# Performance work log

Hardware: AMD Instinct MI355X
Metric: run time of the kernel (lower is better)

Reference implementation:

```python
import jax, jax.numpy as jnp
import numpy as np

N, F, C, H, E, G, L = 50000, 128, 64, 4, 500000, 32, 4
EPS = 1e-5
NEG_SLOPE = 0.2


def setup_inputs() -> dict:
    key = jax.random.key(0)
    ks = jax.random.split(key, 16)
    x = jax.random.normal(ks[0], (N, F), dtype=jnp.float32)
    edge_index = jax.random.randint(ks[1], (2, E), 0, N, dtype=jnp.int64)
    batch = jnp.sort(jax.random.randint(ks[2], (N,), 0, G, dtype=jnp.int64))
    s = 0.05
    params = {
        'Wp': jax.random.normal(ks[3], (F, C), jnp.float32) * s,          # initial_proj (no bias)
        'Wl': jax.random.normal(ks[4], (L, C, H * C), jnp.float32) * s,   # GATv2 lin_l per layer
        'bl': jax.random.normal(ks[5], (L, H * C), jnp.float32) * s,
        'Wr': jax.random.normal(ks[6], (L, C, H * C), jnp.float32) * s,   # GATv2 lin_r per layer
        'br': jax.random.normal(ks[7], (L, H * C), jnp.float32) * s,
        'att': jax.random.normal(ks[8], (L, H, C), jnp.float32) * s,      # attention vector per head
        'cb': jax.random.normal(ks[9], (L, C), jnp.float32) * s,          # conv output bias (concat=False)
        'ln_w': jnp.ones((L, C), jnp.float32),                            # pyg LayerNorm affine
        'ln_b': jnp.zeros((L, C), jnp.float32),
        'Wh': jax.random.normal(ks[10], (C, 1), jnp.float32) * s,         # head
        'bh': jnp.zeros((1,), jnp.float32),
    }
    return {'x': x, 'edge_index': edge_index, 'batch': batch, **params}


def _gatv2(x, src, dst, Wl, bl, Wr, br, att, cb):
    # x: [N, C] -> per-head projections [N, H, C]
    xl = (x @ Wl + bl).reshape(N, H, C)
    xr = (x @ Wr + br).reshape(N, H, C)
    # edge-wise GATv2 scores: leaky_relu(x_i + x_j) . att   -> [E, H]
    e = jax.nn.leaky_relu(xl[src] + xr[dst], NEG_SLOPE)
    score = jnp.einsum('ehc,hc->eh', e, att)
    # segment softmax over incoming edges of each destination node
    m = jax.ops.segment_max(score, dst, num_segments=N)[dst]
    p = jnp.exp(score - m)
    denom = jax.ops.segment_sum(p, dst, num_segments=N)[dst]
    alpha = p / denom                                     # [E, H]
    msg = xl[src] * alpha[..., None]                      # [E, H, C]
    out = jax.ops.segment_sum(msg, dst, num_segments=N)   # [N, H, C]
    return out.mean(axis=1) + cb                          # concat=False: head mean + bias


def _graph_norm(x, w, b):
    # pyg.nn.LayerNorm mode='graph' with batch=None: normalize over ALL elements
    xc = x - x.mean()
    std = jnp.sqrt(xc.var())
    return (xc / (std + EPS)) * w + b


def reference(x, edge_index, batch, Wp, Wl, bl, Wr, br, att, cb, ln_w, ln_b, Wh, bh):
    src, dst = edge_index[0], edge_index[1]
    h = x @ Wp
    for l in range(L):
        h = _gatv2(h, src, dst, Wl[l], bl[l], Wr[l], br[l], att[l], cb[l])
        h = jax.nn.selu(_graph_norm(h, ln_w[l], ln_b[l]))
    # global mean pool over graphs
    counts = jax.ops.segment_sum(jnp.ones((N,), h.dtype), batch, num_segments=G)
    pooled = jax.ops.segment_sum(h, batch, num_segments=G) / jnp.maximum(counts, 1.0)[:, None]
    return (pooled @ Wh + bh).squeeze(-1)  # [G]
```

## Files before the change

### kernel.cpp

```cpp
#include <hip/hip_runtime.h>
#include <hip/hip_bf16.h>
#include <hip/hip_fp8.h>
#include <math.h>

#define NN 50000
#define FIN 128
#define CC 64
#define HH 4
#define HC 256
#define EE 500000
#define GG 32
#define LL 4

typedef __hip_bfloat16 bf16;
typedef __attribute__((ext_vector_type(2))) float f2;
typedef __attribute__((ext_vector_type(8))) short s8v;
typedef __attribute__((ext_vector_type(4))) float f4v;

__device__ __forceinline__ float b2f(bf16 v){ return __bfloat162float(v); }
__device__ __forceinline__ bf16 f2b(float v){ return __float2bfloat16(v); }
__device__ __forceinline__ void unpack2(unsigned u, float& a, float& b){
  union { unsigned q; float f; } x, y;
  x.q = u << 16; y.q = u & 0xffff0000u; a = x.f; b = y.f;
}
__device__ __forceinline__ f2 unpackf2(unsigned u){
  union { unsigned q; float f; } x, y;
  x.q = u << 16; y.q = u & 0xffff0000u;
  f2 r; r.x = x.f; r.y = y.f; return r;
}
__device__ __forceinline__ f2 maxf2(f2 a, f2 b){
#if __has_builtin(__builtin_elementwise_max)
  return __builtin_elementwise_max(a, b);
#else
  f2 r; r.x = fmaxf(a.x, b.x); r.y = fmaxf(a.y, b.y); return r;
#endif
}
__device__ __forceinline__ float clamp4(float v){ return fminf(fmaxf(v, -1e4f), 1e4f); }
__device__ __forceinline__ unsigned pack2bf(float a, float b){
  bf16 x = f2b(clamp4(a)), y = f2b(clamp4(b));
  unsigned short ux = *(unsigned short*)&x, uy = *(unsigned short*)&y;
  return (unsigned)ux | ((unsigned)uy << 16);
}
__device__ __forceinline__ unsigned f4_to_fp8x4(float a, float b, float c, float d){
  a = fminf(fmaxf(a, -240.f), 240.f);
  b = fminf(fmaxf(b, -240.f), 240.f);
  c = fminf(fmaxf(c, -240.f), 240.f);
  d = fminf(fmaxf(d, -240.f), 240.f);
#if __has_builtin(__builtin_amdgcn_cvt_pk_fp8_f32)
  int p = 0;
  p = __builtin_amdgcn_cvt_pk_fp8_f32(a, b, p, false);
  p = __builtin_amdgcn_cvt_pk_fp8_f32(c, d, p, true);
  return (unsigned)p;
#else
  __hip_fp8_e4m3 qa(a), qb(b), qc(c), qd(d);
  return (unsigned)qa.__x | ((unsigned)qb.__x << 8) | ((unsigned)qc.__x << 16) | ((unsigned)qd.__x << 24);
#endif
}
__device__ __forceinline__ void fp8x4_to_f2(unsigned u, f2& lo, f2& hi){
#if __has_builtin(__builtin_amdgcn_cvt_pk_f32_fp8)
  lo = __builtin_amdgcn_cvt_pk_f32_fp8((int)u, false);
  hi = __builtin_amdgcn_cvt_pk_f32_fp8((int)u, true);
#else
  __hip_fp8_e4m3 q0, q1, q2, q3;
  q0.__x = u & 0xff; q1.__x = (u >> 8) & 0xff; q2.__x = (u >> 16) & 0xff; q3.__x = (u >> 24) & 0xff;
  lo.x = (float)q0; lo.y = (float)q1; hi.x = (float)q2; hi.y = (float)q3;
#endif
}
__device__ __forceinline__ float selu_f(float y){
  const float SS = 1.0507009873554805f, SA = 1.6732632423543772f;
  return y > 0.f ? SS*y : SS*SA*(__expf(y) - 1.f);
}
__device__ __forceinline__ int ld_i(const void* p, int i, int w8){
  if (w8) return (int)((const long long*)p)[i];
  return ((const int*)p)[i];
}
__device__ __forceinline__ void stats_inline(const float* __restrict__ partials, float& mu, float& inv){
  float s1 = 0.f, s2 = 0.f;
  #pragma unroll 8
  for (int i = 0; i < 64; ++i){ s1 += partials[i]; s2 += partials[64 + i]; }
  float cnt = (float)NN * 64.f;
  mu = s1 / cnt;
  float var = s2 / cnt - mu*mu;
  if (!(var > 0.f)) var = 0.f;
  inv = 1.0f / (sqrtf(var) + 1e-5f);
}

__global__ __launch_bounds__(256) void k_setup(
    const void* ei, const void* batch,
    const void* Wp, const void* Wl, const void* bl, const void* Wr, const void* br,
    const void* att, const void* cb, const void* lnw, const void* lnb,
    const void* Wh, const void* bh,
    float* dst, int* deg, float* pooled, int* flags, short* apack){
  int b = blockIdx.x;
  int t = threadIdx.x;
  const unsigned short* lw = (const unsigned short*)lnw;
  int f32 = (lw[0] == 0x0000 && lw[1] == 0x3F80) ? 1 : 0;
  if (b < 560){
    int i = b*256 + t;
    if (i < 143169){
      const void* src; int idx;
      if      (i < 8192)   { src = Wp;  idx = i; }
      else if (i < 73728)  { src = Wl;  idx = i - 8192; }
      else if (i < 74752)  { src = bl;  idx = i - 73728; }
      else if (i < 140288) { src = Wr;  idx = i - 74752; }
      else if (i < 141312) { src = br;  idx = i - 140288; }
      else if (i < 142336) { src = att; idx = i - 141312; }
      else if (i < 142592) { src = cb;  idx = i - 142336; }
      else if (i < 142848) { src = lnw; idx = i - 142592; }
      else if (i < 143104) { src = lnb; idx = i - 142848; }
      else if (i < 143168) { src = Wh;  idx = i - 143104; }
      else                 { src = bh;  idx = 0; }
      dst[i] = f32 ? ((const float*)src)[idx] : b2f(((const bf16*)src)[idx]);
    }
  } else if (b < 756){
    int i = (b - 560)*256 + t;
    if (i < NN) deg[i] = 0;
  } else if (b == 756){
    for (int i = t; i < GG*64; i += 256) pooled[i] = 0.f;
    if (t < 64){
      int lane = t;
      const int* w  = (const int*)ei;
      const int* wb = (const int*)batch;
      int bad_e = (lane < 32) ? (w[2*(lane*15625) + 1] != 0) : 0;
      int bad_b = (lane < 32) ? (wb[25001 + 2*lane] != 0) : 0;
      unsigned long long me = __ballot(bad_e);
      unsigned long long mb = __ballot(bad_b);
      if (lane == 0){
        flags[0] = (me == 0ULL) ? 1 : 0;
        flags[1] = (mb == 0ULL) ? 1 : 0;
        flags[2] = f32;
      }
    }
  } else {
    int i2 = (b - 757)*256 + t;
    int l   = i2 >> 15;
    int rem = i2 & 32767;
    int ct  = rem >> 10;
    int rem2 = rem & 1023;
    int kh  = rem2 >> 9;
    int li  = (rem2 >> 3) & 63;
    int j   = rem2 & 7;
    int k   = kh*32 + ((li >> 4) << 3) + j;
    int c   = (ct << 4) + (li & 15);
    const void* Wsrc = (c < 256) ? Wl : Wr;
    int cc = c & 255;
    size_t idx = ((size_t)l*64 + k)*256 + cc;
    float v = f32 ? ((const float*)Wsrc)[idx] : b2f(((const bf16*)Wsrc)[idx]);
    bf16 bv = f2b(v);
    apack[i2] = *(short*)&bv;
  }
}

__global__ __launch_bounds__(256) void k_hist(const void* __restrict__ ei, int* __restrict__ deg,
                                              const int* __restrict__ flags){
  int e = blockIdx.x*256 + threadIdx.x;
  if (e < EE){
    int d = ld_i(ei, EE + e, flags[0]);
    if ((unsigned)d < NN) atomicAdd(&deg[d], 1);
  }
}

__global__ __launch_bounds__(256) void k_scan1(const int* __restrict__ deg, int* __restrict__ off,
                                               int* __restrict__ btot){
  int t = threadIdx.x;
  int i = blockIdx.x*256 + t;
  int v = (i < NN) ? deg[i] : 0;
  int incl = v;
  #pragma unroll
  for (int dl = 1; dl < 64; dl <<= 1){
    int u = __shfl_up(incl, dl, 64);
    if ((t & 63) >= dl) incl += u;
  }
  __shared__ int wt[4];
  if ((t & 63) == 63) wt[t >> 6] = incl;
  __syncthreads();
  int base = 0;
  for (int ww = 0; ww < (t >> 6); ++ww) base += wt[ww];
  incl += base;
  if (i < NN) off[i + 1] = incl;
  if (t == 255) btot[blockIdx.x] = incl;
}

__global__ __launch_bounds__(256) void k_scan2(const int* __restrict__ btot, int* __restrict__ boff, int nb){
  int t = threadIdx.x;
  int v = (t < nb) ? btot[t] : 0;
  int incl = v;
  #pragma unroll
  for (int dl = 1; dl < 64; dl <<= 1){
    int u = __shfl_up(incl, dl, 64);
    if ((t & 63) >= dl) incl += u;
  }
  __shared__ int wt[4];
  if ((t & 63) == 63) wt[t >> 6] = incl;
  __syncthreads();
  int base = 0;
  for (int ww = 0; ww < (t >> 6); ++ww) base += wt[ww];
  incl += base;
  if (t < 256) boff[t] = incl - v;
}

__global__ __launch_bounds__(256) void k_scan3(int* __restrict__ off, int* __restrict__ cursor,
                                               const int* __restrict__ deg, const int* __restrict__ boff){
  int i = blockIdx.x*256 + threadIdx.x;
  if (i >= NN) return;
  int v = off[i + 1] + boff[i >> 8];
  off[i + 1] = v;
  cursor[i] = v - deg[i];
  if (i == 0) off[0] = 0;
}

__global__ __launch_bounds__(256) void k_scatter_gb(const void* __restrict__ ei, int* __restrict__ cursor,
                                                    int* __restrict__ ssrc, const void* __restrict__ batch,
                                                    int* __restrict__ gstart, const int* __restrict__ flags){
  int b = blockIdx.x;
  if (b < 1954){
    int e = b*256 + threadIdx.x;
    if (e < EE){
      int f = flags[0];
      int s = ld_i(ei, e, f);
      int d = ld_i(ei, EE + e, f);
      if ((unsigned)d < NN && (unsigned)s < NN){
        int p = atomicAdd(&cursor[d], 1);
        ssrc[p] = s << 8;
      }
    }
  } else {
    int i = (b - 1954)*256 + threadIdx.x;
    if (i >= NN) return;
    int f = flags[1];
    int bb = ld_i(batch, i, f);
    bb = min(max(bb, 0), GG - 1);
    if (i == 0){ for (int q = 0; q <= bb; ++q) gstart[q] = 0; }
    else {
      int pb = ld_i(batch, i - 1, f);
      pb = min(max(pb, 0), GG - 1);
      for (int q = pb + 1; q <= bb; ++q) gstart[q] = i;
    }
    if (i == NN - 1){ for (int q = bb + 1; q <= GG; ++q) gstart[q] = NN; }
  }
}

__global__ __launch_bounds__(256) void k_proj(const void* __restrict__ xraw, const float* __restrict__ Wp32,
                                              float* __restrict__ h, const int* __restrict__ flags){
  __shared__ float xs[64*128];
  __shared__ float wsm[128*64];
  int t = threadIdx.x;
  int r0 = blockIdx.x * 64;
  int rows = NN - r0; if (rows > 64) rows = 64;
  const float4* gw = (const float4*)Wp32;
  #pragma unroll
  for (int i = 0; i < 8; ++i) ((float4*)wsm)[i*256 + t] = gw[i*256 + t];
  int f32 = flags[2];
  #pragma unroll
  for (int i = 0; i < 8; ++i){
    int p = i*256 + t;
    int r = p >> 5, kq = p & 31;
    float4 v = make_float4(0.f,0.f,0.f,0.f);
    if (r < rows){
      if (f32) v = ((const float4*)xraw)[(size_t)(r0 + r)*32 + kq];
      else {
        uint2 u = ((const uint2*)xraw)[(size_t)(r0 + r)*32 + kq];
        unpack2(u.x, v.x, v.y); unpack2(u.y, v.z, v.w);
      }
    }
    *(float4*)&xs[r*128 + kq*4] = v;
  }
  __syncthreads();
  int tx = t & 15, ty = t >> 4;
  int c0 = tx*4, rr0 = ty*4;
  float acc[4][4] = {{0.f}};
  for (int k = 0; k < 128; k += 4){
    float4 xv[4];
    #pragma unroll
    for (int i = 0; i < 4; ++i) xv[i] = *(const float4*)&xs[(rr0 + i)*128 + k];
    const float* xf = (const float*)xv;
    #pragma unroll
    for (int m = 0; m < 4; ++m){
      float4 wv = *(const float4*)&wsm[(k + m)*64 + c0];
      #pragma unroll
      for (int i = 0; i < 4; ++i){
        float xm = xf[i*4 + m];
        acc[i][0] = fmaf(xm, wv.x, acc[i][0]);
        acc[i][1] = fmaf(xm, wv.y, acc[i][1]);
        acc[i][2] = fmaf(xm, wv.z, acc[i][2]);
        acc[i][3] = fmaf(xm, wv.w, acc[i][3]);
      }
    }
  }
  #pragma unroll
  for (int i = 0; i < 4; ++i){
    int r = rr0 + i;
    if (r < rows){
      float4 o;
      o.x = clamp4(acc[i][0]); o.y = clamp4(acc[i][1]);
      o.z = clamp4(acc[i][2]); o.w = clamp4(acc[i][3]);
      *(float4*)&h[(size_t)(r0 + r)*64 + c0] = o;
    }
  }
}

__global__ __launch_bounds__(256) void k_gemm2m(const float* __restrict__ h,
    const s8v* __restrict__ apack,
    const float* __restrict__ bl, const float* __restrict__ br,
    unsigned char* __restrict__ xl8, bf16* __restrict__ xr,
    const float* __restrict__ partials, const float* __restrict__ lnw, const float* __restrict__ lnb,
    int apply){
  __shared__ short buf[64*264];
  int t = threadIdx.x;
  int r0 = blockIdx.x * 64;
  int rows = NN - r0; if (rows > 64) rows = 64;
  float mu = 0.f, inv = 0.f;
  if (apply) stats_inline(partials, mu, inv);
  #pragma unroll
  for (int i = 0; i < 4; ++i){
    int p = i*256 + t;
    int r = p >> 4, kq = p & 15;
    uint2 pk; pk.x = 0u; pk.y = 0u;
    if (r < rows){
      float4 v = ((const float4*)h)[(size_t)(r0 + r)*16 + kq];
      if (apply){
        float4 w4 = *(const float4*)(lnw + kq*4);
        float4 b4 = *(const float4*)(lnb + kq*4);
        v.x = selu_f((v.x - mu)*inv*w4.x + b4.x);
        v.y = selu_f((v.y - mu)*inv*w4.y + b4.y);
        v.z = selu_f((v.z - mu)*inv*w4.z + b4.z);
        v.w = selu_f((v.w - mu)*inv*w4.w + b4.w);
      }
      pk.x = pack2bf(v.x, v.y);
      pk.y = pack2bf(v.z, v.w);
    }
    *(uint2*)&buf[r*264 + kq*4] = pk;
  }
  __syncthreads();
  int wave = t >> 6, lane = t & 63;
  int n = lane & 15, q = lane >> 4;
  int rowb = wave * 16;
  s8v bf0 = *(const s8v*)&buf[(rowb + n)*264 + q*8];
  s8v bf1 = *(const s8v*)&buf[(rowb + n)*264 + 32 + q*8];
  __syncthreads();
  {
    unsigned* ubuf = (unsigned*)buf;
    #pragma unroll 4
    for (int cc = 0; cc < 16; ++cc){
      s8v a0 = apack[cc*128 + lane];
      s8v a1 = apack[cc*128 + 64 + lane];
      f4v acc = {0.f, 0.f, 0.f, 0.f};
      acc = __builtin_amdgcn_mfma_f32_16x16x32_bf16(a0, bf0, acc, 0, 0, 0);
      acc = __builtin_amdgcn_mfma_f32_16x16x32_bf16(a1, bf1, acc, 0, 0, 0);
      int colh = (cc << 4) + (q << 2);
      float4 bb = *(const float4*)&bl[colh];
      ubuf[(rowb + n)*132 + (colh >> 2)] =
          f4_to_fp8x4(acc[0] + bb.x, acc[1] + bb.y, acc[2] + bb.z, acc[3] + bb.w);
    }
    __syncthreads();
    #pragma unroll
    for (int i = 0; i < 16; ++i){
      int idx = i*256 + t;
      int row = idx >> 6, colu = idx & 63;
      if (row < rows){
        unsigned v = ubuf[row*132 + colu];
        ((unsigned*)xl8)[((size_t)(r0 + row))*64 + colu] = v;
      }
    }
    __syncthreads();
  }
  {
    #pragma unroll 4
    for (int cc = 0; cc < 16; ++cc){
      int ct = 16 + cc;
      s8v a0 = apack[ct*128 + lane];
      s8v a1 = apack[ct*128 + 64 + lane];
      f4v acc = {0.f, 0.f, 0.f, 0.f};
      acc = __builtin_amdgcn_mfma_f32_16x16x32_bf16(a0, bf0, acc, 0, 0, 0);
      acc = __builtin_amdgcn_mfma_f32_16x16x32_bf16(a1, bf1, acc, 0, 0, 0);
      int colh = (cc << 4) + (q << 2);
      float4 bb = *(const float4*)&br[colh];
      uint2 pk;
      pk.x = pack2bf(acc[0] + bb.x, acc[1] + bb.y);
      pk.y = pack2bf(acc[2] + bb.z, acc[3] + bb.w);
      *(uint2*)&buf[(rowb + n)*264 + colh] = pk;
    }
    __syncthreads();
    #pragma unroll
    for (int i = 0; i < 16; ++i){
      int idx = i*256 + t;
      int row = idx >> 6, col = idx & 63;
      if (row < rows){
        uint2 v = *(const uint2*)&buf[row*264 + col*4];
        *(uint2*)&xr[((size_t)(r0 + row))*256 + col*4] = v;
      }
    }
  }
}

__global__ __launch_bounds__(256) void k_gat(const unsigned char* __restrict__ xl8, const bf16* __restrict__ xr,
    const int* __restrict__ off, const int* __restrict__ ssrc,
    const float* __restrict__ att, const float* __restrict__ cbp,
    float* __restrict__ out, float2* __restrict__ nstat){
  int t = threadIdx.x;
  int wave = t >> 6, lane = t & 63;
  int d = blockIdx.x*4 + wave;
  if (d >= NN) return;
  int s0 = off[d], s1 = off[d + 1];
  int head = lane >> 4;
  int c4 = (lane & 15) * 4;

  float4 av4 = *(const float4*)(att + head*64 + c4);
  f2 av01; av01.x = av4.x; av01.y = av4.y;
  f2 av23; av23.x = av4.z; av23.y = av4.w;
  uint2 ur = *(const uint2*)(xr + (size_t)d * 256 + lane*4);
  f2 r01 = unpackf2(ur.x), r23 = unpackf2(ur.y);
  const float NS = 0.2f;

  float denom = 0.f;
  f2 m01; m01.x = 0.f; m01.y = 0.f;
  f2 m23; m23.x = 0.f; m23.y = 0.f;
  int e = s0;
  for (; e + 1 < s1; e += 2){
    int ofa = ssrc[e];
    int ofb = ssrc[e + 1];
    unsigned ua = *(const unsigned*)(xl8 + (size_t)(unsigned)ofa + lane*4);
    unsigned ub = *(const unsigned*)(xl8 + (size_t)(unsigned)ofb + lane*4);
    f2 xa01, xa23, xb01, xb23;
    fp8x4_to_f2(ua, xa01, xa23);
    fp8x4_to_f2(ub, xb01, xb23);
    f2 ta01 = xa01 + r01, ta23 = xa23 + r23;
    f2 tb01 = xb01 + r01, tb23 = xb23 + r23;
    ta01 = maxf2(ta01, ta01*NS); ta23 = maxf2(ta23, ta23*NS);
    tb01 = maxf2(tb01, tb01*NS); tb23 = maxf2(tb23, tb23*NS);
    f2 sa2 = av01*ta01 + av23*ta23;
    f2 sb2 = av01*tb01 + av23*tb23;
    float sa = sa2.x + sa2.y;
    float sb = sb2.x + sb2.y;
    sa += __shfl_xor(sa, 1, 64); sb += __shfl_xor(sb, 1, 64);
    sa += __shfl_xor(sa, 2, 64); sb += __shfl_xor(sb, 2, 64);
    sa += __shfl_xor(sa, 4, 64); sb += __shfl_xor(sb, 4, 64);
    sa += __shfl_xor(sa, 8, 64); sb += __shfl_xor(sb, 8, 64);
    float pa = __expf(fminf(sa, 30.f));
    float pb = __expf(fminf(sb, 30.f));
    denom += pa + pb;
    m01 = m01 + xa01*pa + xb01*pb;
    m23 = m23 + xa23*pa + xb23*pb;
  }
  if (e < s1){
    int ofa = ssrc[e];
    unsigned ua = *(const unsigned*)(xl8 + (size_t)(unsigned)ofa + lane*4);
    f2 xa01, xa23;
    fp8x4_to_f2(ua, xa01, xa23);
    f2 ta01 = xa01 + r01, ta23 = xa23 + r23;
    ta01 = maxf2(ta01, ta01*NS); ta23 = maxf2(ta23, ta23*NS);
    f2 sa2 = av01*ta01 + av23*ta23;
    float sa = sa2.x + sa2.y;
    sa += __shfl_xor(sa, 1, 64); sa += __shfl_xor(sa, 2, 64);
    sa += __shfl_xor(sa, 4, 64); sa += __shfl_xor(sa, 8, 64);
    float pa = __expf(fminf(sa, 30.f));
    denom += pa;
    m01 = m01 + xa01*pa;
    m23 = m23 + xa23*pa;
  }
  float inv = denom > 0.f ? 1.0f / denom : 0.f;
  float v0 = m01.x*inv, v1 = m01.y*inv, v2 = m23.x*inv, v3 = m23.y*inv;
  v0 += __shfl_xor(v0, 16, 64); v1 += __shfl_xor(v1, 16, 64);
  v2 += __shfl_xor(v2, 16, 64); v3 += __shfl_xor(v3, 16, 64);
  v0 += __shfl_xor(v0, 32, 64); v1 += __shfl_xor(v1, 32, 64);
  v2 += __shfl_xor(v2, 32, 64); v3 += __shfl_xor(v3, 32, 64);
  if (lane < 16){
    float4 cbv = *(const float4*)(cbp + c4);
    float4 o;
    o.x = clamp4(0.25f*v0 + cbv.x); o.y = clamp4(0.25f*v1 + cbv.y);
    o.z = clamp4(0.25f*v2 + cbv.z); o.w = clamp4(0.25f*v3 + cbv.w);
    ((float4*)(out + (size_t)d * 64))[lane] = o;
    float s1p = o.x + o.y + o.z + o.w;
    float s2p = o.x*o.x + o.y*o.y + o.z*o.z + o.w*o.w;
    s1p += __shfl_xor(s1p, 1, 64); s2p += __shfl_xor(s2p, 1, 64);
    s1p += __shfl_xor(s1p, 2, 64); s2p += __shfl_xor(s2p, 2, 64);
    s1p += __shfl_xor(s1p, 4, 64); s2p += __shfl_xor(s2p, 4, 64);
    s1p += __shfl_xor(s1p, 8, 64); s2p += __shfl_xor(s2p, 8, 64);
    if (lane == 0){
      float2 ns; ns.x = s1p; ns.y = s2p;
      nstat[d] = ns;
    }
  }
}

__global__ __launch_bounds__(256) void k_nstat(const float2* __restrict__ nstat, float* __restrict__ partials){
  int t = threadIdx.x;
  int gid = blockIdx.x*256 + t;
  float s1 = 0.f, s2 = 0.f;
  for (int i = gid; i < NN; i += 64*256){
    float2 v = nstat[i];
    s1 += v.x; s2 += v.y;
  }
  #pragma unroll
  for (int dl = 1; dl < 64; dl <<= 1){ s1 += __shfl_xor(s1, dl, 64); s2 += __shfl_xor(s2, dl, 64); }
  __shared__ float l1[4], l2[4];
  int w = t >> 6;
  if ((t & 63) == 0){ l1[w] = s1; l2[w] = s2; }
  __syncthreads();
  if (t == 0){
    partials[blockIdx.x]      = l1[0] + l1[1] + l1[2] + l1[3];
    partials[64 + blockIdx.x] = l2[0] + l2[1] + l2[2] + l2[3];
  }
}

__global__ __launch_bounds__(256) void k_poolA(const float* __restrict__ h, const void* __restrict__ batch,
                                               float* __restrict__ pooled, const int* __restrict__ flags,
                                               const float* __restrict__ partials,
                                               const float* __restrict__ lnw, const float* __restrict__ lnb){
  int t = threadIdx.x;
  int c = t & 63, rq = t >> 6;
  int r0 = blockIdx.x * 256;
  int r1 = r0 + 256; if (r1 > NN) r1 = NN;
  int f = flags[1];
  float mu, inv;
  stats_inline(partials, mu, inv);
  float wc = lnw[c], bc = lnb[c];
  float acc = 0.f;
  int cur_g = -1;
  for (int r = r0 + rq; r < r1; r += 4){
    int g = ld_i(batch, r, f);
    g = min(max(g, 0), GG - 1);
    if (g != cur_g){
      if (cur_g >= 0) atomicAdd(&pooled[cur_g*64 + c], acc);
      acc = 0.f; cur_g = g;
    }
    acc += selu_f((h[(size_t)r*64 + c] - mu)*inv*wc + bc);
  }
  if (cur_g >= 0) atomicAdd(&pooled[cur_g*64 + c], acc);
}

__global__ __launch_bounds__(64) void k_poolB(const float* __restrict__ pooled, const int* __restrict__ gstart,
    const float* __restrict__ Wh, const float* __restrict__ bh, void* __restrict__ outp,
    const int* __restrict__ flags){
  int g = blockIdx.x, t = threadIdx.x;
  int rs = gstart[g], re = gstart[g + 1];
  int cnt = re - rs; if (cnt < 1) cnt = 1;
  float val = (pooled[g*64 + t] / (float)cnt) * Wh[t];
  #pragma unroll
  for (int dl = 1; dl < 64; dl <<= 1) val += __shfl_xor(val, dl, 64);
  if (t == 0){
    float res = val + bh[0];
    if (flags[2]) ((float*)outp)[g] = res;
    else          ((bf16*)outp)[g] = f2b(res);
  }
}

extern "C" void kernel_launch(void* const* d_in, const int* in_sizes, int n_in,
                              void* d_out, int out_size, void* d_ws, size_t ws_size,
                              hipStream_t stream) {
  const void* x     = d_in[0];
  const void* ei    = d_in[1];
  const void* batch = d_in[2];
  const void* Wp    = d_in[3];
  const void* Wl    = d_in[4];
  const void* bl    = d_in[5];
  const void* Wr    = d_in[6];
  const void* br    = d_in[7];
  const void* att   = d_in[8];
  const void* cb    = d_in[9];
  const void* lnw   = d_in[10];
  const void* lnb   = d_in[11];
  const void* Wh    = d_in[12];
  const void* bh    = d_in[13];

  char* w = (char*)d_ws;
  int*   flags  = (int*)w;     w += 256;
  int*   deg    = (int*)w;     w += 200192;
  int*   off    = (int*)w;     w += 200192;
  int*   cursor = (int*)w;     w += 200192;
  int*   btot   = (int*)w;     w += 1024;
  int*   boff   = (int*)w;     w += 1024;
  int*   gstart = (int*)w;     w += 256;
  float* partials = (float*)w; w += 2048;
  float* pooled = (float*)w;   w += GG*64*4;
  float* wcvt   = (float*)w;   w += 572928;
  short* apack  = (short*)w;   w += 262144;
  float2* nstat = (float2*)w;  w += (size_t)NN*8;
  int*   ssrc   = (int*)w;     w += (size_t)EE*4;
  float* hbuf   = (float*)w;   w += (size_t)NN*64*4;
  unsigned char* xlb = (unsigned char*)w; w += (size_t)NN*256;
  bf16*  xrb    = (bf16*)w;    w += (size_t)NN*256*2;

  float* Wp32  = wcvt;
  float* bl32  = wcvt + 73728;
  float* br32  = wcvt + 140288;
  float* att32 = wcvt + 141312;
  float* cb32  = wcvt + 142336;
  float* lnw32 = wcvt + 142592;
  float* lnb32 = wcvt + 142848;
  float* Wh32  = wcvt + 143104;
  float* bh32  = wcvt + 143168;

  const int NB = (NN + 255) / 256;
  const int NT = (NN + 63) / 64;

  k_setup<<<757 + 512, 256, 0, stream>>>(ei, batch, Wp, Wl, bl, Wr, br, att, cb, lnw, lnb, Wh, bh,
                                         wcvt, deg, pooled, flags, apack);
  k_hist<<<(EE + 255)/256, 256, 0, stream>>>(ei, deg, flags);
  k_scan1<<<NB, 256, 0, stream>>>(deg, off, btot);
  k_scan2<<<1, 256, 0, stream>>>(btot, boff, NB);
  k_scan3<<<NB, 256, 0, stream>>>(off, cursor, deg, boff);
  k_scatter_gb<<<1954 + NB, 256, 0, stream>>>(ei, cursor, ssrc, batch, gstart, flags);

  k_proj<<<NT, 256, 0, stream>>>(x, Wp32, hbuf, flags);

  for (int l = 0; l < LL; ++l){
    int lp = (l > 0) ? (l - 1) : 0;
    k_gemm2m<<<NT, 256, 0, stream>>>(hbuf,
        (const s8v*)(apack + (size_t)l*32768),
        bl32 + (size_t)l*256, br32 + (size_t)l*256, xlb, xrb,
        partials, lnw32 + (size_t)lp*CC, lnb32 + (size_t)lp*CC, l > 0 ? 1 : 0);
    k_gat<<<(NN + 3)/4, 256, 0, stream>>>(xlb, xrb, off, ssrc,
        att32 + (size_t)l*HH*CC, cb32 + (size_t)l*CC, hbuf, nstat);
    k_nstat<<<64, 256, 0, stream>>>(nstat, partials);
  }

  k_poolA<<<NB, 256, 0, stream>>>(hbuf, batch, pooled, flags, partials,
      lnw32 + (size_t)3*CC, lnb32 + (size_t)3*CC);
  k_poolB<<<GG, 64, 0, stream>>>(pooled, gstart, Wh32, bh32, d_out, flags);
}
```

Measured before the change: 512.3 us.

## Restructure GAT kernel with persistent atomic work queue and two-edge-per-wave lanes

The GATv2 aggregation kernel becomes persistent. Waves grab four destination nodes at a time from an atomic counter kept in the flags array, which setup zeroes. Each half-wave handles one edge, with every lane covering 8 channels. Source indices are loaded cooperatively per 64-edge chunk and broadcast with shuffles, and xl loads are software-pipelined two steps ahead. Leaky-relu is rewritten algebraically as 0.6*x+0.4*|x|, which shortens the score shuffle reduction. The aim is better load balance, more memory-level parallelism, and fewer shuffles and index loads per edge, at the cost of atomic contention and some idle lanes on low-degree nodes.

```diff
diff --git a/kernel.cpp b/kernel.cpp
--- a/kernel.cpp
+++ b/kernel.cpp
@@ -69,6 +69,9 @@
 __device__ __forceinline__ float selu_f(float y){
   const float SS = 1.0507009873554805f, SA = 1.6732632423543772f;
   return y > 0.f ? SS*y : SS*SA*(__expf(y) - 1.f);
+}
+__device__ __forceinline__ f2 shxor_f2(f2 v, int m){
+  f2 r; r.x = __shfl_xor(v.x, m, 64); r.y = __shfl_xor(v.y, m, 64); return r;
 }
 __device__ __forceinline__ int ld_i(const void* p, int i, int w8){
   if (w8) return (int)((const long long*)p)[i];
@@ -117,6 +120,7 @@
     if (i < NN) deg[i] = 0;
   } else if (b == 756){
     for (int i = t; i < GG*64; i += 256) pooled[i] = 0.f;
+    if (t >= 8 && t < 16) flags[t] = 0;
     if (t < 64){
       int lane = t;
       const int* w  = (const int*)ei;
@@ -396,89 +400,113 @@
 __global__ __launch_bounds__(256) void k_gat(const unsigned char* __restrict__ xl8, const bf16* __restrict__ xr,
     const int* __restrict__ off, const int* __restrict__ ssrc,
     const float* __restrict__ att, const float* __restrict__ cbp,
-    float* __restrict__ out, float2* __restrict__ nstat){
-  int t = threadIdx.x;
-  int wave = t >> 6, lane = t & 63;
-  int d = blockIdx.x*4 + wave;
-  if (d >= NN) return;
-  int s0 = off[d], s1 = off[d + 1];
-  int head = lane >> 4;
-  int c4 = (lane & 15) * 4;
-
-  float4 av4 = *(const float4*)(att + head*64 + c4);
-  f2 av01; av01.x = av4.x; av01.y = av4.y;
-  f2 av23; av23.x = av4.z; av23.y = av4.w;
-  uint2 ur = *(const uint2*)(xr + (size_t)d * 256 + lane*4);
-  f2 r01 = unpackf2(ur.x), r23 = unpackf2(ur.y);
-  const float NS = 0.2f;
-
-  float denom = 0.f;
-  f2 m01; m01.x = 0.f; m01.y = 0.f;
-  f2 m23; m23.x = 0.f; m23.y = 0.f;
-  int e = s0;
-  for (; e + 1 < s1; e += 2){
-    int ofa = ssrc[e];
-    int ofb = ssrc[e + 1];
-    unsigned ua = *(const unsigned*)(xl8 + (size_t)(unsigned)ofa + lane*4);
-    unsigned ub = *(const unsigned*)(xl8 + (size_t)(unsigned)ofb + lane*4);
-    f2 xa01, xa23, xb01, xb23;
-    fp8x4_to_f2(ua, xa01, xa23);
-    fp8x4_to_f2(ub, xb01, xb23);
-    f2 ta01 = xa01 + r01, ta23 = xa23 + r23;
-    f2 tb01 = xb01 + r01, tb23 = xb23 + r23;
-    ta01 = maxf2(ta01, ta01*NS); ta23 = maxf2(ta23, ta23*NS);
-    tb01 = maxf2(tb01, tb01*NS); tb23 = maxf2(tb23, tb23*NS);
-    f2 sa2 = av01*ta01 + av23*ta23;
-    f2 sb2 = av01*tb01 + av23*tb23;
-    float sa = sa2.x + sa2.y;
-    float sb = sb2.x + sb2.y;
-    sa += __shfl_xor(sa, 1, 64); sb += __shfl_xor(sb, 1, 64);
-    sa += __shfl_xor(sa, 2, 64); sb += __shfl_xor(sb, 2, 64);
-    sa += __shfl_xor(sa, 4, 64); sb += __shfl_xor(sb, 4, 64);
-    sa += __shfl_xor(sa, 8, 64); sb += __shfl_xor(sb, 8, 64);
-    float pa = __expf(fminf(sa, 30.f));
-    float pb = __expf(fminf(sb, 30.f));
-    denom += pa + pb;
-    m01 = m01 + xa01*pa + xb01*pb;
-    m23 = m23 + xa23*pa + xb23*pb;
-  }
-  if (e < s1){
-    int ofa = ssrc[e];
-    unsigned ua = *(const unsigned*)(xl8 + (size_t)(unsigned)ofa + lane*4);
-    f2 xa01, xa23;
-    fp8x4_to_f2(ua, xa01, xa23);
-    f2 ta01 = xa01 + r01, ta23 = xa23 + r23;
-    ta01 = maxf2(ta01, ta01*NS); ta23 = maxf2(ta23, ta23*NS);
-    f2 sa2 = av01*ta01 + av23*ta23;
-    float sa = sa2.x + sa2.y;
-    sa += __shfl_xor(sa, 1, 64); sa += __shfl_xor(sa, 2, 64);
-    sa += __shfl_xor(sa, 4, 64); sa += __shfl_xor(sa, 8, 64);
-    float pa = __expf(fminf(sa, 30.f));
-    denom += pa;
-    m01 = m01 + xa01*pa;
-    m23 = m23 + xa23*pa;
-  }
-  float inv = denom > 0.f ? 1.0f / denom : 0.f;
-  float v0 = m01.x*inv, v1 = m01.y*inv, v2 = m23.x*inv, v3 = m23.y*inv;
-  v0 += __shfl_xor(v0, 16, 64); v1 += __shfl_xor(v1, 16, 64);
-  v2 += __shfl_xor(v2, 16, 64); v3 += __shfl_xor(v3, 16, 64);
-  v0 += __shfl_xor(v0, 32, 64); v1 += __shfl_xor(v1, 32, 64);
-  v2 += __shfl_xor(v2, 32, 64); v3 += __shfl_xor(v3, 32, 64);
-  if (lane < 16){
-    float4 cbv = *(const float4*)(cbp + c4);
-    float4 o;
-    o.x = clamp4(0.25f*v0 + cbv.x); o.y = clamp4(0.25f*v1 + cbv.y);
-    o.z = clamp4(0.25f*v2 + cbv.z); o.w = clamp4(0.25f*v3 + cbv.w);
-    ((float4*)(out + (size_t)d * 64))[lane] = o;
-    float s1p = o.x + o.y + o.z + o.w;
-    float s2p = o.x*o.x + o.y*o.y + o.z*o.z + o.w*o.w;
-    s1p += __shfl_xor(s1p, 1, 64); s2p += __shfl_xor(s2p, 1, 64);
-    s1p += __shfl_xor(s1p, 2, 64); s2p += __shfl_xor(s2p, 2, 64);
-    s1p += __shfl_xor(s1p, 4, 64); s2p += __shfl_xor(s2p, 4, 64);
-    s1p += __shfl_xor(s1p, 8, 64); s2p += __shfl_xor(s2p, 8, 64);
-    if (lane == 0){
-      float2 ns; ns.x = s1p; ns.y = s2p;
-      nstat[d] = ns;
+    float* __restrict__ out, float2* __restrict__ nstat,
+    int* __restrict__ flags, int layer){
+  int lane = threadIdx.x & 63;
+  int half = lane >> 5;
+  int l5 = lane & 31;
+  int hh = l5 >> 3;
+  int ch0 = (l5 & 7) * 8;
+  const float* ap = att + hh*64 + ch0;
+  float4 avA = *(const float4*)ap;
+  float4 avB = *(const float4*)(ap + 4);
+  int* ctr = flags + 8 + layer;
+  for (;;){
+    int d0 = 0;
+    if (lane == 0) d0 = atomicAdd(ctr, 4);
+    d0 = __shfl(d0, 0, 64);
+    if (d0 >= NN) break;
+    int dend = d0 + 4; if (dend > NN) dend = NN;
+    for (int d = d0; d < dend; ++d){
+      int s0 = off[d];
+      int nd = off[d + 1] - s0;
+      uint4 urw = *(const uint4*)((const unsigned char*)xr + (size_t)d*512 + ((unsigned)l5 << 4));
+      f2 r01 = unpackf2(urw.x), r23 = unpackf2(urw.y), r45 = unpackf2(urw.z), r67 = unpackf2(urw.w);
+      float den = 0.f;
+      f2 m01 = {0.f,0.f}, m23 = {0.f,0.f}, m45 = {0.f,0.f}, m67 = {0.f,0.f};
+      for (int base = 0; base < nd; base += 64){
+        int chunk = nd - base; if (chunk > 64) chunk = 64;
+        int sreg = 0;
+        if (lane < chunk) sreg = ssrc[s0 + base + lane];
+        auto ldpair = [&](int k)->uint2 {
+          int idc = k + half; idc = (idc < chunk) ? idc : (chunk - 1);
+          int of = __shfl(sreg, idc, 64);
+          return *(const uint2*)(xl8 + (size_t)(unsigned)of + ((unsigned)l5 << 3));
+        };
+        uint2 bufA = ldpair(0);
+        uint2 bufB = bufA;
+        if (chunk > 2) bufB = ldpair(2);
+        for (int k = 0; k < chunk; k += 2){
+          uint2 nxt = bufB;
+          if (k + 4 < chunk) nxt = ldpair(k + 4);
+          f2 x01, x23, x45, x67;
+          fp8x4_to_f2(bufA.x, x01, x23);
+          fp8x4_to_f2(bufA.y, x45, x67);
+          f2 t01 = x01 + r01, t23 = x23 + r23, t45 = x45 + r45, t67 = x67 + r67;
+          float lin = t01.x * avA.x;
+          lin = fmaf(t01.y, avA.y, lin);
+          lin = fmaf(t23.x, avA.z, lin);
+          lin = fmaf(t23.y, avA.w, lin);
+          lin = fmaf(t45.x, avB.x, lin);
+          lin = fmaf(t45.y, avB.y, lin);
+          lin = fmaf(t67.x, avB.z, lin);
+          lin = fmaf(t67.y, avB.w, lin);
+          float ab = fabsf(t01.x) * avA.x;
+          ab = fmaf(fabsf(t01.y), avA.y, ab);
+          ab = fmaf(fabsf(t23.x), avA.z, ab);
+          ab = fmaf(fabsf(t23.y), avA.w, ab);
+          ab = fmaf(fabsf(t45.x), avB.x, ab);
+          ab = fmaf(fabsf(t45.y), avB.y, ab);
+          ab = fmaf(fabsf(t67.x), avB.z, ab);
+          ab = fmaf(fabsf(t67.y), avB.w, ab);
+          float s = 0.6f*lin + 0.4f*ab;
+          s += __shfl_xor(s, 1, 64);
+          s += __shfl_xor(s, 2, 64);
+          s += __shfl_xor(s, 4, 64);
+          float p = __expf(fminf(s, 30.f));
+          p = ((k + half) < chunk) ? p : 0.f;
+          den += p;
+          m01 += x01 * p; m23 += x23 * p; m45 += x45 * p; m67 += x67 * p;
+          bufA = bufB; bufB = nxt;
+        }
+      }
+      den += __shfl_xor(den, 32, 64);
+      m01 = m01 + shxor_f2(m01, 32);
+      m23 = m23 + shxor_f2(m23, 32);
+      m45 = m45 + shxor_f2(m45, 32);
+      m67 = m67 + shxor_f2(m67, 32);
+      float iv = den > 0.f ? 1.0f / den : 0.f;
+      f2 v01 = m01 * iv, v23 = m23 * iv, v45 = m45 * iv, v67 = m67 * iv;
+      v01 = v01 + shxor_f2(v01, 8);  v23 = v23 + shxor_f2(v23, 8);
+      v45 = v45 + shxor_f2(v45, 8);  v67 = v67 + shxor_f2(v67, 8);
+      v01 = v01 + shxor_f2(v01, 16); v23 = v23 + shxor_f2(v23, 16);
+      v45 = v45 + shxor_f2(v45, 16); v67 = v67 + shxor_f2(v67, 16);
+      if (lane < 8){
+        float4 cba = *(const float4*)(cbp + lane*8);
+        float4 cbb = *(const float4*)(cbp + lane*8 + 4);
+        float4 oA, oB;
+        oA.x = clamp4(0.25f*v01.x + cba.x);
+        oA.y = clamp4(0.25f*v01.y + cba.y);
+        oA.z = clamp4(0.25f*v23.x + cba.z);
+        oA.w = clamp4(0.25f*v23.y + cba.w);
+        oB.x = clamp4(0.25f*v45.x + cbb.x);
+        oB.y = clamp4(0.25f*v45.y + cbb.y);
+        oB.z = clamp4(0.25f*v67.x + cbb.z);
+        oB.w = clamp4(0.25f*v67.y + cbb.w);
+        float4* orow = (float4*)(out + (size_t)d*64);
+        orow[lane*2]     = oA;
+        orow[lane*2 + 1] = oB;
+        float s1p = oA.x + oA.y + oA.z + oA.w + oB.x + oB.y + oB.z + oB.w;
+        float s2p = oA.x*oA.x + oA.y*oA.y + oA.z*oA.z + oA.w*oA.w
+                  + oB.x*oB.x + oB.y*oB.y + oB.z*oB.z + oB.w*oB.w;
+        s1p += __shfl_xor(s1p, 1, 64); s2p += __shfl_xor(s2p, 1, 64);
+        s1p += __shfl_xor(s1p, 2, 64); s2p += __shfl_xor(s2p, 2, 64);
+        s1p += __shfl_xor(s1p, 4, 64); s2p += __shfl_xor(s2p, 4, 64);
+        if (lane == 0){
+          float2 ns; ns.x = s1p; ns.y = s2p;
+          nstat[d] = ns;
+        }
+      }
     }
   }
 }
@@ -610,8 +638,8 @@
         (const s8v*)(apack + (size_t)l*32768),
         bl32 + (size_t)l*256, br32 + (size_t)l*256, xlb, xrb,
         partials, lnw32 + (size_t)lp*CC, lnb32 + (size_t)lp*CC, l > 0 ? 1 : 0);
-    k_gat<<<(NN + 3)/4, 256, 0, stream>>>(xlb, xrb, off, ssrc,
-        att32 + (size_t)l*HH*CC, cb32 + (size_t)l*CC, hbuf, nstat);
+    k_gat<<<2048, 256, 0, stream>>>(xlb, xrb, off, ssrc,
+        att32 + (size_t)l*HH*CC, cb32 + (size_t)l*CC, hbuf, nstat, flags, l);
     k_nstat<<<64, 256, 0, stream>>>(nstat, partials);
   }
 
```

Measured after the change: 1.319 ms. +157.6%, slower.
